# Kernel tuning notes

Measured on AMD Instinct MI355X. Metric: run time of the kernel, lower is better.

Reference implementation:

```python
import jax, jax.numpy as jnp
import numpy as np

B, S, D, H, Dh, F = 1, 2048, 2048, 24, 128, 8192  # batch, seq, dim, heads, dim_head, ff hidden
SCALE = Dh ** -0.5


def _layernorm(x, g, b, eps=1e-5):
    mu = jnp.mean(x, axis=-1, keepdims=True)
    var = jnp.var(x, axis=-1, keepdims=True)
    return (x - mu) * jax.lax.rsqrt(var + eps) * g + b


def _rmsnorm(x, g, eps=1e-5):
    ms = jnp.mean(jnp.square(x), axis=-1, keepdims=True)
    return x * jax.lax.rsqrt(ms + eps) * g


def setup_inputs() -> dict:
    key = jax.random.key(0)
    ks = jax.random.split(key, 8)
    w = lambda k, sh: (jax.random.normal(k, sh, jnp.float32) * (1.0 / np.sqrt(sh[0]))).astype(jnp.float32)
    return {
        "x": jax.random.normal(ks[0], (B, S, D), jnp.float32),
        "ln_g": jnp.ones((D,), jnp.float32),
        "ln_b": jnp.zeros((D,), jnp.float32),
        "attn_g": jnp.ones((D,), jnp.float32),  # RingAttention prenorm (RMSNorm) gamma
        "Wq": w(ks[1], (D, H * Dh)),
        "Wk": w(ks[2], (D, H * Dh)),
        "Wv": w(ks[3], (D, H * Dh)),
        "Wo": w(ks[4], (H * Dh, D)),
        "W1": w(ks[5], (D, F)),
        "b1": jnp.zeros((F,), jnp.float32),
        "W2": w(ks[6], (F, D)),
        "b2": jnp.zeros((D,), jnp.float32),
    }


def reference(x, ln_g, ln_b, attn_g, Wq, Wk, Wv, Wo, W1, b1, W2, b2):
    # outer block LayerNorm
    x = _layernorm(x, ln_g, ln_b)

    # --- causal multi-head attention (math-equivalent to ring attention) ---
    h = _rmsnorm(x, attn_g)  # attention's internal prenorm
    q = (h @ Wq).reshape(B, S, H, Dh)
    k = (h @ Wk).reshape(B, S, H, Dh)
    v = (h @ Wv).reshape(B, S, H, Dh)
    scores = jnp.einsum("bqhd,bkhd->bhqk", q, k) * SCALE  # [B,H,S,S]
    causal = jnp.tril(jnp.ones((S, S), bool))
    scores = jnp.where(causal, scores, jnp.finfo(scores.dtype).min)
    attn = jax.nn.softmax(scores, axis=-1)
    o = jnp.einsum("bhqk,bkhd->bqhd", attn, v).reshape(B, S, H * Dh)
    x = o @ Wo + x  # residual

    # --- feedforward + residual ---
    x = jax.nn.gelu(x @ W1 + b1) @ W2 + b2 + x
    return x
```

## Files before the change

### kernel.cpp

```cpp
#include <hip/hip_runtime.h>
#include <hip/hip_bf16.h>

#define Sq 2048
#define Dm 2048
#define HDim 3072
#define QKVDim 9216
#define NH 24
#define DH 128
#define FF 8192
#define ATT_SCALE 0.08838834764831845f

using bf16 = __hip_bfloat16;
typedef __attribute__((ext_vector_type(8))) short bf16x8;
typedef __attribute__((ext_vector_type(4))) float f32x4;
typedef unsigned int u32;
typedef unsigned long long u64;
typedef __attribute__((ext_vector_type(4))) u32 u32x4;

__device__ __forceinline__ void gload_lds16(const void* g, void* l) {
    __builtin_amdgcn_global_load_lds(
        (const __attribute__((address_space(1))) void*)g,
        (__attribute__((address_space(3))) void*)l, 16, 0, 0);
}

__global__ __launch_bounds__(256) void ln_rms_kernel(
    const float* __restrict__ x, const float* __restrict__ g, const float* __restrict__ b,
    const float* __restrict__ ag, float* __restrict__ xnf, bf16* __restrict__ h)
{
    __shared__ float redA[4], redB[4], redC[4];
    int row = blockIdx.x;
    int t = threadIdx.x;
    int lane = t & 63, wid = t >> 6;
    const float* xr = x + (size_t)row * Dm;

    float v[8];
    float sum = 0.f, ssq = 0.f;
#pragma unroll
    for (int i = 0; i < 8; i++) {
        float f = xr[t + 256 * i];
        v[i] = f; sum += f; ssq += f * f;
    }
#pragma unroll
    for (int off = 32; off > 0; off >>= 1) {
        sum += __shfl_down(sum, off);
        ssq += __shfl_down(ssq, off);
    }
    if (lane == 0) { redA[wid] = sum; redB[wid] = ssq; }
    __syncthreads();
    sum = redA[0] + redA[1] + redA[2] + redA[3];
    ssq = redB[0] + redB[1] + redB[2] + redB[3];
    float mu = sum * (1.f / Dm);
    float var = ssq * (1.f / Dm) - mu * mu;
    float rstd = rsqrtf(var + 1e-5f);

    float xn[8];
    float s2 = 0.f;
#pragma unroll
    for (int i = 0; i < 8; i++) {
        int col = t + 256 * i;
        float xv = (v[i] - mu) * rstd * g[col] + b[col];
        xn[i] = xv;
        xnf[(size_t)row * Dm + col] = xv;
        s2 += xv * xv;
    }
#pragma unroll
    for (int off = 32; off > 0; off >>= 1) s2 += __shfl_down(s2, off);
    if (lane == 0) redC[wid] = s2;
    __syncthreads();
    s2 = redC[0] + redC[1] + redC[2] + redC[3];
    float rms = rsqrtf(s2 * (1.f / Dm) + 1e-5f);
#pragma unroll
    for (int i = 0; i < 8; i++) {
        int col = t + 256 * i;
        h[(size_t)row * Dm + col] = __float2bfloat16(xn[i] * rms * ag[col]);
    }
}

__global__ __launch_bounds__(256) void transpose_cvt_kernel(
    const float* __restrict__ W, bf16* __restrict__ Wt, int K, int N)
{
    __shared__ float tile[32][36];
    int n0 = blockIdx.x * 32, k0 = blockIdx.y * 32;
    int t = threadIdx.x;
    int r = t >> 3, c4 = (t & 7) * 4;
    f32x4 v = *reinterpret_cast<const f32x4*>(W + (size_t)(k0 + r) * N + n0 + c4);
    *reinterpret_cast<f32x4*>(&tile[r][c4]) = v;
    __syncthreads();
    int nr = t >> 3, kc = (t & 7) * 4;
    bf16 o4[4];
    o4[0] = __float2bfloat16(tile[kc + 0][nr]);
    o4[1] = __float2bfloat16(tile[kc + 1][nr]);
    o4[2] = __float2bfloat16(tile[kc + 2][nr]);
    o4[3] = __float2bfloat16(tile[kc + 3][nr]);
    *reinterpret_cast<u64*>(Wt + (size_t)(n0 + nr) * K + k0 + kc) = *reinterpret_cast<const u64*>(o4);
}

__global__ __launch_bounds__(256) void cvt_bf16_kernel(
    const float* __restrict__ in, bf16* __restrict__ o, int n)
{
    int i = (blockIdx.x * 256 + threadIdx.x) * 8;
    if (i >= n) return;
    f32x4 a = *reinterpret_cast<const f32x4*>(in + i);
    f32x4 b = *reinterpret_cast<const f32x4*>(in + i + 4);
    bf16 r[8];
#pragma unroll
    for (int j = 0; j < 4; j++) { r[j] = __float2bfloat16(a[j]); r[4 + j] = __float2bfloat16(b[j]); }
    *reinterpret_cast<u32x4*>(o + i) = *reinterpret_cast<const u32x4*>(r);
}

__global__ __launch_bounds__(256) void prefill_kernel(
    const float* __restrict__ resid, const float* __restrict__ bias,
    float* __restrict__ o, int N)
{
    int i = (blockIdx.x * 256 + threadIdx.x) * 4;
    int col = i % N;
    f32x4 r = *reinterpret_cast<const f32x4*>(resid + i);
    f32x4 b = *reinterpret_cast<const f32x4*>(bias + col);
    f32x4 ov = {r[0] + b[0], r[1] + b[1], r[2] + b[2], r[3] + b[3]};
    *reinterpret_cast<f32x4*>(o + i) = ov;
}

template <int EPI>
__global__ __launch_bounds__(256, 4) void gemm_kernel(
    const bf16* __restrict__ A, const bf16* __restrict__ Bt,
    int M, int N, int K, int Ksplit,
    bf16* Cb, float* Cf, const float* __restrict__ bias)
{
    __shared__ __align__(16) bf16 As[128 * 64];
    __shared__ __align__(16) bf16 Bs[128 * 64];
    int m0 = blockIdx.y * 128, n0 = blockIdx.x * 128;
    int kbeg = blockIdx.z * Ksplit, kend = kbeg + Ksplit;
    int tid = threadIdx.x;
    int lane = tid & 63, w = tid >> 6;
    int wr = w >> 1, wc = w & 1;
    int l15 = lane & 15, lhi = lane >> 4;

    int srow = lane >> 3;
    int scol = ((lane & 7) ^ (lane >> 3)) * 8;

    const f32x4 zero4 = {0.f, 0.f, 0.f, 0.f};
    f32x4 acc[4][4];
#pragma unroll
    for (int m = 0; m < 4; m++)
#pragma unroll
        for (int n = 0; n < 4; n++) acc[m][n] = zero4;

    for (int k0 = kbeg; k0 < kend; k0 += 64) {
        __syncthreads();
#pragma unroll
        for (int c = 0; c < 4; c++) {
            int row = w * 32 + c * 8 + srow;
            gload_lds16(A + (size_t)(m0 + row) * K + k0 + scol,
                        (char*)As + w * 4096 + c * 1024);
            gload_lds16(Bt + (size_t)(n0 + row) * K + k0 + scol,
                        (char*)Bs + w * 4096 + c * 1024);
        }
        __syncthreads();
#pragma unroll
        for (int ks = 0; ks < 2; ks++) {
            bf16x8 af[4], bfr[4];
#pragma unroll
            for (int m = 0; m < 4; m++) {
                int r = wr * 64 + m * 16 + l15;
                af[m] = *reinterpret_cast<const bf16x8*>(
                    &As[r * 64 + (((ks << 2) + lhi) ^ (r & 7)) * 8]);
            }
#pragma unroll
            for (int n = 0; n < 4; n++) {
                int r = wc * 64 + n * 16 + l15;
                bfr[n] = *reinterpret_cast<const bf16x8*>(
                    &Bs[r * 64 + (((ks << 2) + lhi) ^ (r & 7)) * 8]);
            }
#pragma unroll
            for (int m = 0; m < 4; m++)
#pragma unroll
                for (int n = 0; n < 4; n++)
                    acc[m][n] = __builtin_amdgcn_mfma_f32_16x16x32_bf16(af[m], bfr[n], acc[m][n], 0, 0, 0);
        }
    }

#pragma unroll
    for (int m = 0; m < 4; m++) {
        int row = m0 + wr * 64 + m * 16 + lhi * 4;
#pragma unroll
        for (int n = 0; n < 4; n++) {
            int col = n0 + wc * 64 + n * 16 + l15;
#pragma unroll
            for (int j = 0; j < 4; j++) {
                float vv = acc[m][n][j];
                size_t idx = (size_t)(row + j) * N + col;
                if (EPI == 0) {
                    Cb[idx] = __float2bfloat16(vv);
                } else if (EPI == 2) {
                    float o = vv + bias[col];
                    float u = 0.7978845608028654f * (o + 0.044715f * o * o * o);
                    Cb[idx] = __float2bfloat16(0.5f * o * (1.0f + tanhf(u)));
                } else {
                    atomicAdd(&Cf[idx], vv);
                }
            }
        }
    }
}

__global__ __launch_bounds__(256) void attn_kernel(
    const bf16* __restrict__ qkv, bf16* __restrict__ o)
{
    __shared__ __align__(16) bf16 KsF[2][64 * 128];
    __shared__ __align__(16) bf16 VtF[2][128 * 72];
    __shared__ __align__(16) bf16 Pl[4][16][72];
    int rank = blockIdx.x;
    int qb = (Sq / 64 - 1) - rank / NH;
    int head = rank % NH;
    const bf16* q = qkv + head * DH;
    const bf16* k = qkv + HDim + head * DH;
    const bf16* v = qkv + 2 * HDim + head * DH;
    int tid = threadIdx.x, lane = tid & 63, w = tid >> 6;
    int l15 = lane & 15, lhi = lane >> 4;
    int qrow0 = qb * 64 + w * 16;

    bf16x8 aq[4];
    const bf16* qbase = q + (size_t)(qrow0 + l15) * QKVDim;
#pragma unroll
    for (int kk = 0; kk < 4; kk++)
        aq[kk] = *reinterpret_cast<const bf16x8*>(qbase + kk * 32 + lhi * 8);

    int krow_st = w * 16;
    int vkv = tid >> 4;
    int vd0 = (tid & 15) * 8;

    const f32x4 zero4 = {0.f, 0.f, 0.f, 0.f};
    f32x4 acc_o[8];
#pragma unroll
    for (int db = 0; db < 8; db++) acc_o[db] = zero4;
    float mrow[4], lrow[4];
#pragma unroll
    for (int r = 0; r < 4; r++) { mrow[r] = -1e30f; lrow[r] = 0.f; }

    {
#pragma unroll
        for (int c = 0; c < 4; c++) {
            int row = krow_st + c * 4 + lhi;
            int cb = l15 ^ (row & 7);
            gload_lds16(k + (size_t)row * QKVDim + cb * 8,
                        (char*)&KsF[0][0] + w * 4096 + c * 1024);
        }
#pragma unroll
        for (int i = 0; i < 4; i++) {
            int kv = vkv + i * 16;
            bf16x8 vv = *reinterpret_cast<const bf16x8*>(v + (size_t)kv * QKVDim + vd0);
            int vb = kv >> 3, kr = kv & 7, xr = (vd0 >> 3) & 7;
#pragma unroll
            for (int j = 0; j < 8; j++)
                VtF[0][(vd0 + j) * 72 + ((vb ^ xr) << 3) + kr] = ((const bf16*)&vv)[j];
        }
        asm volatile("s_waitcnt vmcnt(0)" ::: "memory");
        __syncthreads();
    }

    for (int kb = 0; kb <= qb; kb++) {
        int kv0 = kb * 64;
        int p = kb & 1;
        bf16x8 vreg[4];
        bool pref = (kb < qb);
        if (pref) {
            int nv0 = kv0 + 64;
#pragma unroll
            for (int c = 0; c < 4; c++) {
                int row = krow_st + c * 4 + lhi;
                int cb = l15 ^ (row & 7);
                gload_lds16(k + (size_t)(nv0 + row) * QKVDim + cb * 8,
                            (char*)&KsF[p ^ 1][0] + w * 4096 + c * 1024);
            }
#pragma unroll
            for (int i = 0; i < 4; i++) {
                int kv = vkv + i * 16;
                vreg[i] = *reinterpret_cast<const bf16x8*>(v + (size_t)(nv0 + kv) * QKVDim + vd0);
            }
        }

        f32x4 sacc[4];
#pragma unroll
        for (int nb = 0; nb < 4; nb++) {
            sacc[nb] = zero4;
            int krow = nb * 16 + l15;
#pragma unroll
            for (int kk = 0; kk < 4; kk++) {
                const char* kp = (const char*)&KsF[p][0] + krow * 256 +
                                 ((kk * 64 + lhi * 16) ^ ((krow & 7) << 4));
                bf16x8 bk = *reinterpret_cast<const bf16x8*>(kp);
                sacc[nb] = __builtin_amdgcn_mfma_f32_16x16x32_bf16(aq[kk], bk, sacc[nb], 0, 0, 0);
            }
        }

        bool diag = (kb == qb);
        float sv[4][4];
        float pm[4];
#pragma unroll
        for (int r = 0; r < 4; r++) pm[r] = -1e30f;
#pragma unroll
        for (int nb = 0; nb < 4; nb++) {
            int kvc = kv0 + nb * 16 + l15;
#pragma unroll
            for (int r = 0; r < 4; r++) {
                int qr = qrow0 + lhi * 4 + r;
                float s = sacc[nb][r] * ATT_SCALE;
                if (diag && kvc > qr) s = -1e30f;
                sv[nb][r] = s;
                pm[r] = fmaxf(pm[r], s);
            }
        }
#pragma unroll
        for (int off = 1; off < 16; off <<= 1)
#pragma unroll
            for (int r = 0; r < 4; r++)
                pm[r] = fmaxf(pm[r], __shfl_xor(pm[r], off));

        float ls[4];
#pragma unroll
        for (int r = 0; r < 4; r++) {
            float mnew = fmaxf(mrow[r], pm[r]);
            float sc = __expf(mrow[r] - mnew);
            mrow[r] = mnew;
            lrow[r] *= sc;
#pragma unroll
            for (int db = 0; db < 8; db++) acc_o[db][r] *= sc;
            float lsr = 0.f;
#pragma unroll
            for (int nb = 0; nb < 4; nb++) {
                float pp = __expf(sv[nb][r] - mnew);
                sv[nb][r] = pp;
                lsr += pp;
            }
            ls[r] = lsr;
        }
#pragma unroll
        for (int off = 1; off < 16; off <<= 1)
#pragma unroll
            for (int r = 0; r < 4; r++)
                ls[r] += __shfl_xor(ls[r], off);
#pragma unroll
        for (int r = 0; r < 4; r++) lrow[r] += ls[r];

#pragma unroll
        for (int nb = 0; nb < 4; nb++)
#pragma unroll
            for (int r = 0; r < 4; r++)
                Pl[w][lhi * 4 + r][nb * 16 + l15] = __float2bfloat16(sv[nb][r]);

#pragma unroll
        for (int ks = 0; ks < 2; ks++) {
            bf16x8 ap = *reinterpret_cast<const bf16x8*>(&Pl[w][l15][ks * 32 + lhi * 8]);
#pragma unroll
            for (int db = 0; db < 8; db++) {
                int dv = db * 16 + l15;
                int blk = (ks * 4 + lhi) ^ ((dv >> 3) & 7);
                bf16x8 bv = *reinterpret_cast<const bf16x8*>(&VtF[p][dv * 72 + blk * 8]);
                acc_o[db] = __builtin_amdgcn_mfma_f32_16x16x32_bf16(ap, bv, acc_o[db], 0, 0, 0);
            }
        }

        __syncthreads();
        if (pref) {
#pragma unroll
            for (int i = 0; i < 4; i++) {
                int kv = vkv + i * 16;
                int vb = kv >> 3, kr = kv & 7, xr = (vd0 >> 3) & 7;
#pragma unroll
                for (int j = 0; j < 8; j++)
                    VtF[p ^ 1][(vd0 + j) * 72 + ((vb ^ xr) << 3) + kr] = ((const bf16*)&vreg[i])[j];
            }
            asm volatile("s_waitcnt vmcnt(0)" ::: "memory");
            __syncthreads();
        }
    }

#pragma unroll
    for (int db = 0; db < 8; db++)
#pragma unroll
        for (int r = 0; r < 4; r++) {
            int qr = qrow0 + lhi * 4 + r;
            float val = acc_o[db][r] / lrow[r];
            o[(size_t)qr * HDim + head * DH + db * 16 + l15] = __float2bfloat16(val);
        }
}

extern "C" void kernel_launch(void* const* d_in, const int* in_sizes, int n_in,
                              void* d_out, int out_size, void* d_ws, size_t ws_size,
                              hipStream_t stream)
{
    const float* x     = (const float*)d_in[0];
    const float* ln_g  = (const float*)d_in[1];
    const float* ln_b  = (const float*)d_in[2];
    const float* attng = (const float*)d_in[3];
    const float* Wq    = (const float*)d_in[4];
    const float* Wk    = (const float*)d_in[5];
    const float* Wv    = (const float*)d_in[6];
    const float* Wo    = (const float*)d_in[7];
    const float* W1    = (const float*)d_in[8];
    const float* b1    = (const float*)d_in[9];
    const float* W2    = (const float*)d_in[10];
    const float* b2    = (const float*)d_in[11];
    float* out = (float*)d_out;
    char* ws = (char*)d_ws;

    bf16*  wbuf = (bf16*)(ws + 0);
    float* xnf  = (float*)(ws + 39845888);
    bf16*  hbuf = (bf16*)(ws + 56623104);
    bf16*  qkv  = (bf16*)(ws + 65011712);
    bf16*  ob_  = (bf16*)(ws + 102760448);
    bf16*  gb_  = qkv;

    ln_rms_kernel<<<Sq, 256, 0, stream>>>(x, ln_g, ln_b, attng, xnf, hbuf);

    transpose_cvt_kernel<<<dim3(HDim / 32, Dm / 32), 256, 0, stream>>>(Wq, wbuf, Dm, HDim);
    transpose_cvt_kernel<<<dim3(HDim / 32, Dm / 32), 256, 0, stream>>>(Wk, wbuf + (size_t)HDim * Dm, Dm, HDim);
    transpose_cvt_kernel<<<dim3(HDim / 32, Dm / 32), 256, 0, stream>>>(Wv, wbuf + (size_t)2 * HDim * Dm, Dm, HDim);
    gemm_kernel<0><<<dim3(QKVDim / 128, Sq / 128, 1), 256, 0, stream>>>(
        hbuf, wbuf, Sq, QKVDim, Dm, Dm, qkv, nullptr, nullptr);

    attn_kernel<<<dim3(NH * Sq / 64), 256, 0, stream>>>(qkv, ob_);

    transpose_cvt_kernel<<<dim3(Dm / 32, HDim / 32), 256, 0, stream>>>(Wo, wbuf, HDim, Dm);
    gemm_kernel<4><<<dim3(Dm / 128, Sq / 128, 2), 256, 0, stream>>>(
        ob_, wbuf, Sq, Dm, HDim, HDim / 2, nullptr, xnf, nullptr);
    cvt_bf16_kernel<<<(Sq * Dm) / (256 * 8), 256, 0, stream>>>(xnf, hbuf, Sq * Dm);

    transpose_cvt_kernel<<<dim3(FF / 32, Dm / 32), 256, 0, stream>>>(W1, wbuf, Dm, FF);
    gemm_kernel<2><<<dim3(FF / 128, Sq / 128, 1), 256, 0, stream>>>(
        hbuf, wbuf, Sq, FF, Dm, Dm, gb_, nullptr, b1);

    transpose_cvt_kernel<<<dim3(Dm / 32, FF / 32), 256, 0, stream>>>(W2, wbuf, FF, Dm);
    prefill_kernel<<<(Sq * Dm) / (256 * 4), 256, 0, stream>>>(xnf, b2, out, Dm);
    gemm_kernel<4><<<dim3(Dm / 128, Sq / 128, 2), 256, 0, stream>>>(
        gb_, wbuf, Sq, Dm, FF, FF / 2, nullptr, out, nullptr);
}
```

Baseline: 474.9 us.

## Process two query sub-blocks per attention block, fuse small kernels, cheaper GELU

Each attention block now handles 128 query rows as two 64-row sub-tiles that share every staged K/V tile, halving K/V global loads and LDS staging per query row. Sub-tiles that are fully causal-masked skip their work. The V-transpose thread mapping is also changed. Separately, the three QKV weight transposes become one launch, the bf16 convert and the bias/residual prefill are fused into one pass, and tanh-GELU is rewritten as x*sigmoid(2u) using __expf. Risks are fewer blocks with more causal imbalance in attention, higher register pressure, and slight GELU numeric differences.

Result: slower. 502.6 us (+5.8%).

```diff
diff --git a/kernel.cpp b/kernel.cpp
--- a/kernel.cpp
+++ b/kernel.cpp
@@ -95,29 +95,46 @@
     *reinterpret_cast<u64*>(Wt + (size_t)(n0 + nr) * K + k0 + kc) = *reinterpret_cast<const u64*>(o4);
 }
 
-__global__ __launch_bounds__(256) void cvt_bf16_kernel(
-    const float* __restrict__ in, bf16* __restrict__ o, int n)
+__global__ __launch_bounds__(256) void transpose_cvt3_kernel(
+    const float* __restrict__ Wa, const float* __restrict__ Wb, const float* __restrict__ Wc,
+    bf16* __restrict__ Wt, int K, int N)
+{
+    __shared__ float tile[32][36];
+    const float* W = blockIdx.z == 0 ? Wa : (blockIdx.z == 1 ? Wb : Wc);
+    bf16* dst = Wt + (size_t)blockIdx.z * N * K;
+    int n0 = blockIdx.x * 32, k0 = blockIdx.y * 32;
+    int t = threadIdx.x;
+    int r = t >> 3, c4 = (t & 7) * 4;
+    f32x4 v = *reinterpret_cast<const f32x4*>(W + (size_t)(k0 + r) * N + n0 + c4);
+    *reinterpret_cast<f32x4*>(&tile[r][c4]) = v;
+    __syncthreads();
+    int nr = t >> 3, kc = (t & 7) * 4;
+    bf16 o4[4];
+    o4[0] = __float2bfloat16(tile[kc + 0][nr]);
+    o4[1] = __float2bfloat16(tile[kc + 1][nr]);
+    o4[2] = __float2bfloat16(tile[kc + 2][nr]);
+    o4[3] = __float2bfloat16(tile[kc + 3][nr]);
+    *reinterpret_cast<u64*>(dst + (size_t)(n0 + nr) * K + k0 + kc) = *reinterpret_cast<const u64*>(o4);
+}
+
+__global__ __launch_bounds__(256) void cvt_prefill_kernel(
+    const float* __restrict__ xnf, const float* __restrict__ bias,
+    bf16* __restrict__ hb, float* __restrict__ o, int N)
 {
     int i = (blockIdx.x * 256 + threadIdx.x) * 8;
-    if (i >= n) return;
-    f32x4 a = *reinterpret_cast<const f32x4*>(in + i);
-    f32x4 b = *reinterpret_cast<const f32x4*>(in + i + 4);
+    int col = i % N;
+    f32x4 a = *reinterpret_cast<const f32x4*>(xnf + i);
+    f32x4 b = *reinterpret_cast<const f32x4*>(xnf + i + 4);
     bf16 r[8];
 #pragma unroll
     for (int j = 0; j < 4; j++) { r[j] = __float2bfloat16(a[j]); r[4 + j] = __float2bfloat16(b[j]); }
-    *reinterpret_cast<u32x4*>(o + i) = *reinterpret_cast<const u32x4*>(r);
-}
-
-__global__ __launch_bounds__(256) void prefill_kernel(
-    const float* __restrict__ resid, const float* __restrict__ bias,
-    float* __restrict__ o, int N)
-{
-    int i = (blockIdx.x * 256 + threadIdx.x) * 4;
-    int col = i % N;
-    f32x4 r = *reinterpret_cast<const f32x4*>(resid + i);
-    f32x4 b = *reinterpret_cast<const f32x4*>(bias + col);
-    f32x4 ov = {r[0] + b[0], r[1] + b[1], r[2] + b[2], r[3] + b[3]};
-    *reinterpret_cast<f32x4*>(o + i) = ov;
+    *reinterpret_cast<u32x4*>(hb + i) = *reinterpret_cast<const u32x4*>(r);
+    f32x4 b0 = *reinterpret_cast<const f32x4*>(bias + col);
+    f32x4 b1v = *reinterpret_cast<const f32x4*>(bias + col + 4);
+    f32x4 o0 = {a[0] + b0[0], a[1] + b0[1], a[2] + b0[2], a[3] + b0[3]};
+    f32x4 o1 = {b[0] + b1v[0], b[1] + b1v[1], b[2] + b1v[2], b[3] + b1v[3]};
+    *reinterpret_cast<f32x4*>(o + i) = o0;
+    *reinterpret_cast<f32x4*>(o + i + 4) = o1;
 }
 
 template <int EPI>
@@ -193,8 +210,8 @@
                     Cb[idx] = __float2bfloat16(vv);
                 } else if (EPI == 2) {
                     float o = vv + bias[col];
-                    float u = 0.7978845608028654f * (o + 0.044715f * o * o * o);
-                    Cb[idx] = __float2bfloat16(0.5f * o * (1.0f + tanhf(u)));
+                    float u = 1.5957691216057308f * (o + 0.044715f * o * o * o);
+                    Cb[idx] = __float2bfloat16(o / (1.0f + __expf(-u)));
                 } else {
                     atomicAdd(&Cf[idx], vv);
                 }
@@ -210,32 +227,40 @@
     __shared__ __align__(16) bf16 VtF[2][128 * 72];
     __shared__ __align__(16) bf16 Pl[4][16][72];
     int rank = blockIdx.x;
-    int qb = (Sq / 64 - 1) - rank / NH;
+    int qb = (Sq / 128 - 1) - rank / NH;
     int head = rank % NH;
     const bf16* q = qkv + head * DH;
     const bf16* k = qkv + HDim + head * DH;
     const bf16* v = qkv + 2 * HDim + head * DH;
     int tid = threadIdx.x, lane = tid & 63, w = tid >> 6;
     int l15 = lane & 15, lhi = lane >> 4;
-    int qrow0 = qb * 64 + w * 16;
-
-    bf16x8 aq[4];
-    const bf16* qbase = q + (size_t)(qrow0 + l15) * QKVDim;
-#pragma unroll
-    for (int kk = 0; kk < 4; kk++)
-        aq[kk] = *reinterpret_cast<const bf16x8*>(qbase + kk * 32 + lhi * 8);
+
+    bf16x8 aq[2][4];
+#pragma unroll
+    for (int s = 0; s < 2; s++) {
+        const bf16* qbase = q + (size_t)(qb * 128 + s * 64 + w * 16 + l15) * QKVDim;
+#pragma unroll
+        for (int kk = 0; kk < 4; kk++)
+            aq[s][kk] = *reinterpret_cast<const bf16x8*>(qbase + kk * 32 + lhi * 8);
+    }
 
     int krow_st = w * 16;
-    int vkv = tid >> 4;
-    int vd0 = (tid & 15) * 8;
+    int vkv = lhi * 2 + (w & 1) + (w >> 1) * 8;
+    int vd0 = l15 * 8;
+    int vxr = l15 & 7;
 
     const f32x4 zero4 = {0.f, 0.f, 0.f, 0.f};
-    f32x4 acc_o[8];
-#pragma unroll
-    for (int db = 0; db < 8; db++) acc_o[db] = zero4;
-    float mrow[4], lrow[4];
-#pragma unroll
-    for (int r = 0; r < 4; r++) { mrow[r] = -1e30f; lrow[r] = 0.f; }
+    f32x4 acc_o[2][8];
+    float mrow[2][4], lrow[2][4];
+#pragma unroll
+    for (int s = 0; s < 2; s++) {
+#pragma unroll
+        for (int db = 0; db < 8; db++) acc_o[s][db] = zero4;
+#pragma unroll
+        for (int r = 0; r < 4; r++) { mrow[s][r] = -1e30f; lrow[s][r] = 0.f; }
+    }
+
+    int nt = 2 * qb + 2;
 
     {
 #pragma unroll
@@ -249,20 +274,20 @@
         for (int i = 0; i < 4; i++) {
             int kv = vkv + i * 16;
             bf16x8 vv = *reinterpret_cast<const bf16x8*>(v + (size_t)kv * QKVDim + vd0);
-            int vb = kv >> 3, kr = kv & 7, xr = (vd0 >> 3) & 7;
+            int vb = kv >> 3, kr = kv & 7;
 #pragma unroll
             for (int j = 0; j < 8; j++)
-                VtF[0][(vd0 + j) * 72 + ((vb ^ xr) << 3) + kr] = ((const bf16*)&vv)[j];
+                VtF[0][(vd0 + j) * 72 + ((vb ^ vxr) << 3) + kr] = ((const bf16*)&vv)[j];
         }
         asm volatile("s_waitcnt vmcnt(0)" ::: "memory");
         __syncthreads();
     }
 
-    for (int kb = 0; kb <= qb; kb++) {
+    for (int kb = 0; kb < nt; kb++) {
         int kv0 = kb * 64;
         int p = kb & 1;
         bf16x8 vreg[4];
-        bool pref = (kb < qb);
+        bool pref = (kb + 1 < nt);
         if (pref) {
             int nv0 = kv0 + 64;
 #pragma unroll
@@ -279,96 +304,104 @@
             }
         }
 
-        f32x4 sacc[4];
-#pragma unroll
-        for (int nb = 0; nb < 4; nb++) {
-            sacc[nb] = zero4;
-            int krow = nb * 16 + l15;
-#pragma unroll
-            for (int kk = 0; kk < 4; kk++) {
-                const char* kp = (const char*)&KsF[p][0] + krow * 256 +
-                                 ((kk * 64 + lhi * 16) ^ ((krow & 7) << 4));
-                bf16x8 bk = *reinterpret_cast<const bf16x8*>(kp);
-                sacc[nb] = __builtin_amdgcn_mfma_f32_16x16x32_bf16(aq[kk], bk, sacc[nb], 0, 0, 0);
-            }
-        }
-
-        bool diag = (kb == qb);
-        float sv[4][4];
-        float pm[4];
-#pragma unroll
-        for (int r = 0; r < 4; r++) pm[r] = -1e30f;
-#pragma unroll
-        for (int nb = 0; nb < 4; nb++) {
-            int kvc = kv0 + nb * 16 + l15;
+#pragma unroll
+        for (int s = 0; s < 2; s++) {
+            int qr0s = qb * 128 + s * 64 + w * 16;
+            if (kv0 > qr0s + 15) continue;
+
+            f32x4 sacc[4];
+#pragma unroll
+            for (int nb = 0; nb < 4; nb++) {
+                sacc[nb] = zero4;
+                int krow = nb * 16 + l15;
+#pragma unroll
+                for (int kk = 0; kk < 4; kk++) {
+                    const char* kp = (const char*)&KsF[p][0] + krow * 256 +
+                                     ((kk * 64 + lhi * 16) ^ ((krow & 7) << 4));
+                    bf16x8 bk = *reinterpret_cast<const bf16x8*>(kp);
+                    sacc[nb] = __builtin_amdgcn_mfma_f32_16x16x32_bf16(aq[s][kk], bk, sacc[nb], 0, 0, 0);
+                }
+            }
+
+            bool msk = (kv0 + 63 > qr0s);
+            float sv[4][4];
+            float pm[4];
+#pragma unroll
+            for (int r = 0; r < 4; r++) pm[r] = -1e30f;
+#pragma unroll
+            for (int nb = 0; nb < 4; nb++) {
+                int kvc = kv0 + nb * 16 + l15;
+#pragma unroll
+                for (int r = 0; r < 4; r++) {
+                    int qr = qr0s + lhi * 4 + r;
+                    float ss = sacc[nb][r] * ATT_SCALE;
+                    if (msk && kvc > qr) ss = -1e30f;
+                    sv[nb][r] = ss;
+                    pm[r] = fmaxf(pm[r], ss);
+                }
+            }
+#pragma unroll
+            for (int off = 1; off < 16; off <<= 1)
+#pragma unroll
+                for (int r = 0; r < 4; r++)
+                    pm[r] = fmaxf(pm[r], __shfl_xor(pm[r], off));
+
+            float ls[4];
 #pragma unroll
             for (int r = 0; r < 4; r++) {
-                int qr = qrow0 + lhi * 4 + r;
-                float s = sacc[nb][r] * ATT_SCALE;
-                if (diag && kvc > qr) s = -1e30f;
-                sv[nb][r] = s;
-                pm[r] = fmaxf(pm[r], s);
-            }
-        }
-#pragma unroll
-        for (int off = 1; off < 16; off <<= 1)
-#pragma unroll
-            for (int r = 0; r < 4; r++)
-                pm[r] = fmaxf(pm[r], __shfl_xor(pm[r], off));
-
-        float ls[4];
-#pragma unroll
-        for (int r = 0; r < 4; r++) {
-            float mnew = fmaxf(mrow[r], pm[r]);
-            float sc = __expf(mrow[r] - mnew);
-            mrow[r] = mnew;
-            lrow[r] *= sc;
-#pragma unroll
-            for (int db = 0; db < 8; db++) acc_o[db][r] *= sc;
-            float lsr = 0.f;
-#pragma unroll
-            for (int nb = 0; nb < 4; nb++) {
-                float pp = __expf(sv[nb][r] - mnew);
-                sv[nb][r] = pp;
-                lsr += pp;
-            }
-            ls[r] = lsr;
-        }
-#pragma unroll
-        for (int off = 1; off < 16; off <<= 1)
-#pragma unroll
-            for (int r = 0; r < 4; r++)
-                ls[r] += __shfl_xor(ls[r], off);
-#pragma unroll
-        for (int r = 0; r < 4; r++) lrow[r] += ls[r];
-
-#pragma unroll
-        for (int nb = 0; nb < 4; nb++)
-#pragma unroll
-            for (int r = 0; r < 4; r++)
-                Pl[w][lhi * 4 + r][nb * 16 + l15] = __float2bfloat16(sv[nb][r]);
-
-#pragma unroll
-        for (int ks = 0; ks < 2; ks++) {
-            bf16x8 ap = *reinterpret_cast<const bf16x8*>(&Pl[w][l15][ks * 32 + lhi * 8]);
-#pragma unroll
-            for (int db = 0; db < 8; db++) {
-                int dv = db * 16 + l15;
-                int blk = (ks * 4 + lhi) ^ ((dv >> 3) & 7);
-                bf16x8 bv = *reinterpret_cast<const bf16x8*>(&VtF[p][dv * 72 + blk * 8]);
-                acc_o[db] = __builtin_amdgcn_mfma_f32_16x16x32_bf16(ap, bv, acc_o[db], 0, 0, 0);
+                float mnew = fmaxf(mrow[s][r], pm[r]);
+                float sc = __expf(mrow[s][r] - mnew);
+                mrow[s][r] = mnew;
+                lrow[s][r] *= sc;
+#pragma unroll
+                for (int db = 0; db < 8; db++) acc_o[s][db][r] *= sc;
+                float lsr = 0.f;
+#pragma unroll
+                for (int nb = 0; nb < 4; nb++) {
+                    float pp = __expf(sv[nb][r] - mnew);
+                    sv[nb][r] = pp;
+                    lsr += pp;
+                }
+                ls[r] = lsr;
+            }
+#pragma unroll
+            for (int off = 1; off < 16; off <<= 1)
+#pragma unroll
+                for (int r = 0; r < 4; r++)
+                    ls[r] += __shfl_xor(ls[r], off);
+#pragma unroll
+            for (int r = 0; r < 4; r++) lrow[s][r] += ls[r];
+
+#pragma unroll
+            for (int nb = 0; nb < 4; nb++)
+#pragma unroll
+                for (int r = 0; r < 4; r++)
+                    Pl[w][lhi * 4 + r][nb * 16 + l15] = __float2bfloat16(sv[nb][r]);
+
+#pragma unroll
+            for (int ks = 0; ks < 2; ks++) {
+                bf16x8 ap = *reinterpret_cast<const bf16x8*>(&Pl[w][l15][ks * 32 + lhi * 8]);
+#pragma unroll
+                for (int db = 0; db < 8; db++) {
+                    int dv = db * 16 + l15;
+                    int blk = (ks * 4 + lhi) ^ ((dv >> 3) & 7);
+                    bf16x8 bv = *reinterpret_cast<const bf16x8*>(&VtF[p][dv * 72 + blk * 8]);
+                    acc_o[s][db] = __builtin_amdgcn_mfma_f32_16x16x32_bf16(ap, bv, acc_o[s][db], 0, 0, 0);
+                }
             }
         }
 
         __syncthreads();
         if (pref) {
+            int nv0 = kv0 + 64;
+            (void)nv0;
 #pragma unroll
             for (int i = 0; i < 4; i++) {
                 int kv = vkv + i * 16;
-                int vb = kv >> 3, kr = kv & 7, xr = (vd0 >> 3) & 7;
+                int vb = kv >> 3, kr = kv & 7;
 #pragma unroll
                 for (int j = 0; j < 8; j++)
-                    VtF[p ^ 1][(vd0 + j) * 72 + ((vb ^ xr) << 3) + kr] = ((const bf16*)&vreg[i])[j];
+                    VtF[p ^ 1][(vd0 + j) * 72 + ((vb ^ vxr) << 3) + kr] = ((const bf16*)&vreg[i])[j];
             }
             asm volatile("s_waitcnt vmcnt(0)" ::: "memory");
             __syncthreads();
@@ -376,13 +409,15 @@
     }
 
 #pragma unroll
-    for (int db = 0; db < 8; db++)
-#pragma unroll
-        for (int r = 0; r < 4; r++) {
-            int qr = qrow0 + lhi * 4 + r;
-            float val = acc_o[db][r] / lrow[r];
-            o[(size_t)qr * HDim + head * DH + db * 16 + l15] = __float2bfloat16(val);
-        }
+    for (int s = 0; s < 2; s++)
+#pragma unroll
+        for (int db = 0; db < 8; db++)
+#pragma unroll
+            for (int r = 0; r < 4; r++) {
+                int qr = qb * 128 + s * 64 + w * 16 + lhi * 4 + r;
+                float val = acc_o[s][db][r] / lrow[s][r];
+                o[(size_t)qr * HDim + head * DH + db * 16 + l15] = __float2bfloat16(val);
+            }
 }
 
 extern "C" void kernel_launch(void* const* d_in, const int* in_sizes, int n_in,
@@ -413,25 +448,23 @@
 
     ln_rms_kernel<<<Sq, 256, 0, stream>>>(x, ln_g, ln_b, attng, xnf, hbuf);
 
-    transpose_cvt_kernel<<<dim3(HDim / 32, Dm / 32), 256, 0, stream>>>(Wq, wbuf, Dm, HDim);
-    transpose_cvt_kernel<<<dim3(HDim / 32, Dm / 32), 256, 0, stream>>>(Wk, wbuf + (size_t)HDim * Dm, Dm, HDim);
-    transpose_cvt_kernel<<<dim3(HDim / 32, Dm / 32), 256, 0, stream>>>(Wv, wbuf + (size_t)2 * HDim * Dm, Dm, HDim);
+    transpose_cvt3_kernel<<<dim3(HDim / 32, Dm / 32, 3), 256, 0, stream>>>(
+        Wq, Wk, Wv, wbuf, Dm, HDim);
     gemm_kernel<0><<<dim3(QKVDim / 128, Sq / 128, 1), 256, 0, stream>>>(
         hbuf, wbuf, Sq, QKVDim, Dm, Dm, qkv, nullptr, nullptr);
 
-    attn_kernel<<<dim3(NH * Sq / 64), 256, 0, stream>>>(qkv, ob_);
+    attn_kernel<<<dim3(NH * Sq / 128), 256, 0, stream>>>(qkv, ob_);
 
     transpose_cvt_kernel<<<dim3(Dm / 32, HDim / 32), 256, 0, stream>>>(Wo, wbuf, HDim, Dm);
     gemm_kernel<4><<<dim3(Dm / 128, Sq / 128, 2), 256, 0, stream>>>(
         ob_, wbuf, Sq, Dm, HDim, HDim / 2, nullptr, xnf, nullptr);
-    cvt_bf16_kernel<<<(Sq * Dm) / (256 * 8), 256, 0, stream>>>(xnf, hbuf, Sq * Dm);
+    cvt_prefill_kernel<<<(Sq * Dm) / (256 * 8), 256, 0, stream>>>(xnf, b2, hbuf, out, Dm);
 
     transpose_cvt_kernel<<<dim3(FF / 32, Dm / 32), 256, 0, stream>>>(W1, wbuf, Dm, FF);
     gemm_kernel<2><<<dim3(FF / 128, Sq / 128, 1), 256, 0, stream>>>(
         hbuf, wbuf, Sq, FF, Dm, Dm, gb_, nullptr, b1);
 
     transpose_cvt_kernel<<<dim3(Dm / 32, FF / 32), 256, 0, stream>>>(W2, wbuf, FF, Dm);
-    prefill_kernel<<<(Sq * Dm) / (256 * 4), 256, 0, stream>>>(xnf, b2, out, Dm);
     gemm_kernel<4><<<dim3(Dm / 128, Sq / 128, 2), 256, 0, stream>>>(
         gb_, wbuf, Sq, Dm, FF, FF / 2, nullptr, out, nullptr);
 }
```
